# Kernel tuning notes

Measured on AMD Instinct MI355X. Metric: run time of the kernel, lower is better.

The kernel has to match this reference:

```python
import jax, jax.numpy as jnp
import numpy as np

DMODEL = 1024
N_EXPERTS = 16
EXPERT_SIZE = 256
K = 4


def setup_inputs() -> dict:
    key = jax.random.key(0)
    k1, k2, k3, k4 = jax.random.split(key, 4)
    std_sel = 1.0 / np.sqrt(DMODEL)
    std_val = 1.0 / np.sqrt(N_EXPERTS * EXPERT_SIZE)
    return {
        "x": jax.random.normal(k1, (4, 2048, DMODEL), dtype=jnp.float32),
        "expert_sel": jax.random.normal(k2, (N_EXPERTS, DMODEL), dtype=jnp.float32) * std_sel,
        "keys": jax.random.normal(k3, (N_EXPERTS, DMODEL, EXPERT_SIZE), dtype=jnp.float32) * std_sel,
        "values": jax.random.normal(k4, (N_EXPERTS, EXPERT_SIZE, DMODEL), dtype=jnp.float32) * std_val,
        "route_scale": jnp.ones((1,), dtype=jnp.float32),
    }


def reference(x, expert_sel, keys, values, route_scale):
    # Routing: sigmoid gating, top-k selection (eval mode: no dropout/bias balancing)
    sel_logits = jnp.einsum("btd,ed->bte", x, expert_sel)  # [B,T,E]
    sel_probs = jax.nn.sigmoid(sel_logits)
    _, sel_index = jax.lax.top_k(sel_probs, K)  # [B,T,K]
    sel_val = jnp.take_along_axis(sel_probs, sel_index, axis=-1)  # [B,T,K]
    sel_val = sel_val / jnp.clip(sel_val.sum(-1, keepdims=True), 1e-9)
    sel_val = sel_val * route_scale  # route_scale shape [1] broadcasts
    # Dense all-expert FFN (as in original), then gather top-k and combine
    scores_all = jax.nn.relu(jnp.einsum("btd,edh->bteh", x, keys))  # [B,T,E,H]
    values_all = jnp.einsum("bteh,ehv->btev", scores_all, values)   # [B,T,E,V]
    sel_idx_exp = sel_index[..., None]  # [B,T,K,1]
    selected = jnp.take_along_axis(values_all, sel_idx_exp, axis=2)  # [B,T,K,V]
    out = (selected * sel_val[..., None]).sum(axis=2)  # [B,T,V]
    return out
```

## Files before the change

### kernel.cpp

```cpp
#include <hip/hip_runtime.h>
#include <math.h>


constexpr int NTOK = 8192;
constexpr int DM   = 1024;
constexpr int NE   = 16;
constexpr int EH   = 256;
constexpr int TK   = 4;
constexpr int CAP  = 8192;
constexpr int BM   = 128;

typedef __attribute__((ext_vector_type(8))) short short8;
typedef __attribute__((ext_vector_type(4))) float f32x4;

#define MFMA16(a, b, c) __builtin_amdgcn_mfma_f32_16x16x32_bf16(a, b, c, 0, 0, 0)
#define VMCNT(n) asm volatile("s_waitcnt vmcnt(" #n ")" ::: "memory")
#define LGKM0    asm volatile("s_waitcnt lgkmcnt(0)" ::: "memory")
#define SBAR     __builtin_amdgcn_s_barrier()
#define SCHED0   __builtin_amdgcn_sched_barrier(0)

__device__ __forceinline__ void gload_lds16(const void* g, void* l) {
    __builtin_amdgcn_global_load_lds(
        (const __attribute__((address_space(1))) void*)g,
        (__attribute__((address_space(3))) void*)l, 16, 0, 0);
}

__device__ __forceinline__ unsigned short f2bf(float f) {
    union { float f; unsigned int u; } x; x.f = f;
    unsigned int r = x.u + 0x7fffu + ((x.u >> 16) & 1u);
    return (unsigned short)(r >> 16);
}
__device__ __forceinline__ float bf2f(unsigned short b) {
    union { unsigned int u; float f; } x; x.u = ((unsigned int)b) << 16;
    return x.f;
}

__global__ __launch_bounds__(256) void route_conv_kernel(
    const float* __restrict__ x, const float* __restrict__ esel,
    const float* __restrict__ rscale,
    unsigned short* __restrict__ xb,
    int4* __restrict__ sel4, float* __restrict__ wtk)
{
    __shared__ float Es[NE * DM];
    int tid = threadIdx.x;

    {
        const float4* src = (const float4*)esel;
        float4* dst = (float4*)Es;
        #pragma unroll
        for (int j = 0; j < 16; ++j) dst[tid + j * 256] = src[tid + j * 256];
    }
    __syncthreads();

    int t    = blockIdx.x * 8 + (tid >> 5);
    int l32  = tid & 31;

    float acc[NE];
    #pragma unroll
    for (int e = 0; e < NE; ++e) acc[e] = 0.f;

    const float4* x4 = (const float4*)(x + (size_t)t * DM);
    const float4* E4 = (const float4*)Es;
    #pragma unroll
    for (int i4 = 0; i4 < 8; ++i4) {
        int d4 = i4 * 32 + l32;
        float4 xv = x4[d4];
        ushort4 cb = { f2bf(xv.x), f2bf(xv.y), f2bf(xv.z), f2bf(xv.w) };
        *(ushort4*)(xb + (size_t)t * DM + d4 * 4) = cb;
        #pragma unroll
        for (int e = 0; e < NE; ++e) {
            float4 wv = E4[e * 256 + d4];
            acc[e] = fmaf(xv.x, wv.x, acc[e]);
            acc[e] = fmaf(xv.y, wv.y, acc[e]);
            acc[e] = fmaf(xv.z, wv.z, acc[e]);
            acc[e] = fmaf(xv.w, wv.w, acc[e]);
        }
    }

    #pragma unroll
    for (int off = 16; off; off >>= 1)
        #pragma unroll
        for (int e = 0; e < NE; ++e)
            acc[e] += __shfl_xor(acc[e], off, 32);

    if (l32 == 0) {
        float p[NE];
        #pragma unroll
        for (int e = 0; e < NE; ++e) p[e] = 1.0f / (1.0f + expf(-acc[e]));

        int   sel_e[TK];
        float sel_p[TK];
        float sum = 0.f;
        #pragma unroll
        for (int k = 0; k < TK; ++k) {
            float best = -INFINITY; int be = NE;
            #pragma unroll
            for (int e = 0; e < NE; ++e) {
                bool take = p[e] > best;
                best = take ? p[e] : best;
                be   = take ? e    : be;
            }
            sel_e[k] = be; sel_p[k] = best; sum += best;
            #pragma unroll
            for (int e = 0; e < NE; ++e) p[e] = (e == be) ? -INFINITY : p[e];
        }

        float wsc = rscale[0] / fmaxf(sum, 1e-9f);
        int4 s = { sel_e[0], sel_e[1], sel_e[2], sel_e[3] };
        sel4[t] = s;
        float4 wv = { sel_p[0] * wsc, sel_p[1] * wsc,
                      sel_p[2] * wsc, sel_p[3] * wsc };
        *(float4*)(wtk + t * TK) = wv;
    }
}

__global__ __launch_bounds__(1024) void compact_kernel(
    const int4* __restrict__ sel4, int* __restrict__ counts,
    int* __restrict__ lpk)
{
    __shared__ int wsum[16];
    int e    = blockIdx.x;
    int tid  = threadIdx.x;
    int w    = tid >> 6;
    int lane = tid & 63;

    int base = 0;
    for (int c = 0; c < NTOK; c += 1024) {
        int t = c + tid;
        int4 s = sel4[t];
        int k = -1;
        if      (s.x == e) k = 0;
        else if (s.y == e) k = 1;
        else if (s.z == e) k = 2;
        else if (s.w == e) k = 3;
        unsigned long long m = __ballot(k >= 0);
        int rank = __popcll(m & ((1ull << lane) - 1ull));
        if (lane == 63) wsum[w] = __popcll(m);
        __syncthreads();
        int prefix = 0, total = 0;
        #pragma unroll
        for (int i = 0; i < 16; ++i) {
            int v = wsum[i];
            prefix += (i < w) ? v : 0;
            total  += v;
        }
        if (k >= 0) lpk[e * CAP + base + prefix + rank] = t * TK + k;
        base += total;
        __syncthreads();
    }
    if (tid == 0) counts[e] = base;
}

__global__ __launch_bounds__(256) void trans_kernel(
    const float* __restrict__ in, unsigned short* __restrict__ outp, int R, int C)
{
    __shared__ float T[32][33];
    int e = blockIdx.z;
    int r0 = blockIdx.y * 32, c0 = blockIdx.x * 32;
    int ri = threadIdx.x >> 3, cq = threadIdx.x & 7;
    float4 v = *(const float4*)(in + ((size_t)e * R + r0 + ri) * C + c0 + cq * 4);
    T[ri][cq * 4 + 0] = v.x; T[ri][cq * 4 + 1] = v.y;
    T[ri][cq * 4 + 2] = v.z; T[ri][cq * 4 + 3] = v.w;
    __syncthreads();
    int ci = threadIdx.x >> 3, rq = threadIdx.x & 7;
    ushort4 o = { f2bf(T[rq * 4 + 0][ci]), f2bf(T[rq * 4 + 1][ci]),
                  f2bf(T[rq * 4 + 2][ci]), f2bf(T[rq * 4 + 3][ci]) };
    *(ushort4*)(outp + ((size_t)e * C + c0 + ci) * R + r0 + rq * 4) = o;
}

template<int USE_SCRATCH>
__global__ __launch_bounds__(512, 2) void ffn_kernel(
    const unsigned short* __restrict__ xb,
    const unsigned short* __restrict__ ktb,
    const unsigned short* __restrict__ vtb,
    const int* __restrict__ counts, const int* __restrict__ lpk,
    const float* __restrict__ wtk,
    unsigned short* __restrict__ scratch,
    float* __restrict__ out)
{
    constexpr int BUF  = 24576;
    constexpr int META = 3 * BUF + 65536;
    __shared__ __align__(16) char L[3 * BUF + 65536 + 1536];
    char* const Ss = L + 3 * BUF;
    int*   stok = (int*)(L + META);
    int*   spk  = (int*)(L + META + 512);
    float* sw   = (float*)(L + META + 1024);

    int tid  = threadIdx.x;
    int lane = tid & 63;
    int w    = tid >> 6;
    int lm   = lane & 15;
    int q    = lane >> 4;
    int th   = w >> 2;
    int hq   = w & 3;

    int xp = blockIdx.x & 7;
    int j0 = blockIdx.x >> 3;
    int e0 = xp * 2;
    int c0 = counts[e0], c1 = counts[e0 + 1];
    int n0 = (c0 + BM - 1) >> 7;
    int ntot = n0 + ((c1 + BM - 1) >> 7);

    for (int jt = j0; jt < ntot; jt += 48) {
        int e, t0, cnt;
        if (jt < n0) { e = e0;     t0 = jt << 7;        cnt = c0; }
        else         { e = e0 + 1; t0 = (jt - n0) << 7; cnt = c1; }

        if (tid < BM) {
            int s = t0 + tid;
            if (s < cnt) {
                int pk = lpk[e * CAP + s];
                stok[tid] = pk >> 2; spk[tid] = pk; sw[tid] = wtk[pk];
            } else {
                stok[tid] = 0; spk[tid] = USE_SCRATCH ? (NTOK * TK) : 0; sw[tid] = 0.f;
            }
        }
        LGKM0;
        SBAR;
        SCHED0;

        int rowX = tid >> 2;
        int cb   = ((tid & 3) * 16) ^ (((rowX >> 1) & 3) << 4);
        const unsigned short* kbase = ktb + (size_t)e * EH * DM;
        const unsigned short* vbase = vtb + (size_t)e * DM * EH;
        const unsigned short* srcX  = xb + (size_t)stok[rowX] * DM + (cb >> 1);
        const unsigned short* srcK0 = kbase + (size_t)rowX * DM + (cb >> 1);
        const unsigned short* srcK1 = kbase + (size_t)(rowX + 128) * DM + (cb >> 1);
        const unsigned short* srcV0 = vbase + (size_t)rowX * EH + (cb >> 1);
        const unsigned short* srcV1 = vbase + (size_t)(rowX + 128) * EH + (cb >> 1);

        auto stage1 = [&](char* buf, int kc) {
            gload_lds16(srcX + kc,  buf + w * 1024);
            gload_lds16(srcK0 + kc, buf + 8192 + w * 1024);
            gload_lds16(srcK1 + kc, buf + 16384 + w * 1024);
        };
        auto stageV = [&](char* buf, int nb, int kc) {
            gload_lds16(srcV0 + nb * 256 * EH + kc, buf + w * 1024);
            gload_lds16(srcV1 + nb * 256 * EH + kc, buf + 8192 + w * 1024);
        };

        f32x4 zero = {0.f, 0.f, 0.f, 0.f};
        f32x4 acc[4][4];
        #pragma unroll
        for (int mi = 0; mi < 4; ++mi)
            #pragma unroll
            for (int ni = 0; ni < 4; ++ni) acc[mi][ni] = zero;

        auto comp1 = [&](const char* buf) {
            const char* Kb = buf + 8192;
            short8 a[4], bb[4];
            #pragma unroll
            for (int mi = 0; mi < 4; ++mi) {
                int row = th * 64 + mi * 16 + lm;
                a[mi] = *(const short8*)(buf + row * 64 +
                         ((q * 16) ^ (((row >> 1) & 3) << 4)));
            }
            #pragma unroll
            for (int ni = 0; ni < 4; ++ni) {
                int row = hq * 64 + ni * 16 + lm;
                bb[ni] = *(const short8*)(Kb + row * 64 +
                          ((q * 16) ^ (((row >> 1) & 3) << 4)));
            }
            #pragma unroll
            for (int mi = 0; mi < 4; ++mi)
                #pragma unroll
                for (int ni = 0; ni < 4; ++ni)
                    acc[mi][ni] = MFMA16(a[mi], bb[ni], acc[mi][ni]);
        };

        stage1(L, 0);
        stage1(L + BUF, 32);
        for (int n = 0; n < 30; ++n) {
            VMCNT(3); SBAR; SCHED0;
            stage1(L + ((n + 2) % 3) * BUF, (n + 2) * 32);
            __builtin_amdgcn_s_setprio(1);
            comp1(L + (n % 3) * BUF);
            __builtin_amdgcn_s_setprio(0);
        }
        VMCNT(3); SBAR; SCHED0;
        stageV(L + 2 * BUF, 0, 0);
        __builtin_amdgcn_s_setprio(1);
        comp1(L);
        __builtin_amdgcn_s_setprio(0);
        VMCNT(2); SBAR; SCHED0;
        stageV(L, 0, 32);
        __builtin_amdgcn_s_setprio(1);
        comp1(L + BUF);
        __builtin_amdgcn_s_setprio(0);

        #pragma unroll
        for (int mi = 0; mi < 4; ++mi)
            #pragma unroll
            for (int ni = 0; ni < 4; ++ni) {
                f32x4 v = acc[mi][ni];
                #pragma unroll
                for (int r = 0; r < 4; ++r) {
                    int row = th * 64 + mi * 16 + q * 4 + r;
                    int col = hq * 64 + ni * 16 + lm;
                    *(unsigned short*)(Ss + row * 512 +
                        ((col * 2) ^ ((row & 7) << 4))) = f2bf(fmaxf(v[r], 0.f));
                }
            }
        LGKM0;

        int   spk_[4][4];
        float sw_[4][4];
        int   stok_[4][4];
        #pragma unroll
        for (int mi = 0; mi < 4; ++mi)
            #pragma unroll
            for (int r = 0; r < 4; ++r) {
                int slot = th * 64 + mi * 16 + q * 4 + r;
                spk_[mi][r] = spk[slot];
                if (!USE_SCRATCH) { sw_[mi][r] = sw[slot]; stok_[mi][r] = stok[slot]; }
            }

        for (int nb = 0; nb < 4; ++nb) {
            f32x4 acc2[4][4];
            #pragma unroll
            for (int mi = 0; mi < 4; ++mi)
                #pragma unroll
                for (int ni = 0; ni < 4; ++ni) acc2[mi][ni] = zero;

            #pragma unroll
            for (int j2 = 0; j2 < 8; ++j2) {
                int u = nb * 8 + j2;
                if (u == 31) { VMCNT(0); } else { VMCNT(2); }
                SBAR; SCHED0;
                if (u < 30) {
                    int u2 = u + 2;
                    stageV(L + ((u + 1) % 3) * BUF, u2 >> 3, (u2 & 7) * 32);
                }
                const char* Vb = L + ((u + 2) % 3) * BUF;
                short8 a[4], bb[4];
                #pragma unroll
                for (int mi = 0; mi < 4; ++mi) {
                    int row = th * 64 + mi * 16 + lm;
                    a[mi] = *(const short8*)(Ss + row * 512 +
                             ((j2 * 64 + q * 16) ^ ((row & 7) << 4)));
                }
                #pragma unroll
                for (int ni = 0; ni < 4; ++ni) {
                    int row = hq * 64 + ni * 16 + lm;
                    bb[ni] = *(const short8*)(Vb + row * 64 +
                              ((q * 16) ^ (((row >> 1) & 3) << 4)));
                }
                __builtin_amdgcn_s_setprio(1);
                #pragma unroll
                for (int mi = 0; mi < 4; ++mi)
                    #pragma unroll
                    for (int ni = 0; ni < 4; ++ni)
                        acc2[mi][ni] = MFMA16(a[mi], bb[ni], acc2[mi][ni]);
                __builtin_amdgcn_s_setprio(0);
            }

            #pragma unroll
            for (int mi = 0; mi < 4; ++mi)
                #pragma unroll
                for (int ni = 0; ni < 4; ++ni) {
                    f32x4 v = acc2[mi][ni];
                    #pragma unroll
                    for (int r = 0; r < 4; ++r) {
                        int d = nb * 256 + hq * 64 + ni * 16 + lm;
                        if (USE_SCRATCH) {
                            scratch[(size_t)spk_[mi][r] * DM + d] = f2bf(v[r]);
                        } else {
                            atomicAdd(out + (size_t)stok_[mi][r] * DM + d,
                                      sw_[mi][r] * v[r]);
                        }
                    }
                }
        }
    }
}

__global__ __launch_bounds__(256) void combine_kernel(
    const unsigned short* __restrict__ scratch, const float* __restrict__ wtk,
    float* __restrict__ out)
{
    int t  = blockIdx.x * 2 + (threadIdx.x >> 7);
    int d0 = (threadIdx.x & 127) * 8;
    float o[8] = {0.f, 0.f, 0.f, 0.f, 0.f, 0.f, 0.f, 0.f};
    #pragma unroll
    for (int k = 0; k < TK; ++k) {
        float wv = wtk[t * TK + k];
        uint4 qv = *(const uint4*)(scratch + (size_t)(t * TK + k) * DM + d0);
        unsigned int us[4] = {qv.x, qv.y, qv.z, qv.w};
        #pragma unroll
        for (int j = 0; j < 4; ++j) {
            o[j * 2 + 0] = fmaf(wv, bf2f((unsigned short)(us[j] & 0xffff)), o[j * 2 + 0]);
            o[j * 2 + 1] = fmaf(wv, bf2f((unsigned short)(us[j] >> 16)),    o[j * 2 + 1]);
        }
    }
    float4 w0 = {o[0], o[1], o[2], o[3]}, w1 = {o[4], o[5], o[6], o[7]};
    *(float4*)(out + (size_t)t * DM + d0)     = w0;
    *(float4*)(out + (size_t)t * DM + d0 + 4) = w1;
}

extern "C" void kernel_launch(void* const* d_in, const int* in_sizes, int n_in,
                              void* d_out, int out_size, void* d_ws, size_t ws_size,
                              hipStream_t stream) {
    const float* x      = (const float*)d_in[0];
    const float* esel   = (const float*)d_in[1];
    const float* keys   = (const float*)d_in[2];
    const float* values = (const float*)d_in[3];
    const float* rscale = (const float*)d_in[4];
    float* out = (float*)d_out;

    char* ws = (char*)d_ws;
    size_t o = 0;
    auto alloc = [&](size_t sz) { size_t r = o; o = (o + sz + 255) & ~(size_t)255; return r; };
    size_t o_counts = alloc(NE * 4);
    size_t o_lpk    = alloc((size_t)NE * CAP * 4);
    size_t o_sel4   = alloc((size_t)NTOK * 16);
    size_t o_wtk    = alloc((size_t)NTOK * TK * 4);
    size_t o_xb     = alloc((size_t)NTOK * DM * 2);
    size_t o_ktb    = alloc((size_t)NE * EH * DM * 2);
    size_t o_vtb    = alloc((size_t)NE * DM * EH * 2);
    size_t o_scr    = alloc(((size_t)NTOK * TK + BM) * DM * 2);
    size_t need_full = o;

    int*            counts  = (int*)(ws + o_counts);
    int*            lpk     = (int*)(ws + o_lpk);
    int4*           sel4    = (int4*)(ws + o_sel4);
    float*          wtk     = (float*)(ws + o_wtk);
    unsigned short* xb      = (unsigned short*)(ws + o_xb);
    unsigned short* ktb     = (unsigned short*)(ws + o_ktb);
    unsigned short* vtb     = (unsigned short*)(ws + o_vtb);
    unsigned short* scratch = (unsigned short*)(ws + o_scr);

    bool use_scratch = ws_size >= need_full;

    if (!use_scratch)
        hipMemsetAsync(d_out, 0, (size_t)out_size * sizeof(float), stream);

    route_conv_kernel<<<NTOK / 8, 256, 0, stream>>>(x, esel, rscale, xb,
                                                    sel4, wtk);
    compact_kernel<<<NE, 1024, 0, stream>>>(sel4, counts, lpk);
    trans_kernel<<<dim3(EH / 32, DM / 32, NE), 256, 0, stream>>>(keys, ktb, DM, EH);
    trans_kernel<<<dim3(DM / 32, EH / 32, NE), 256, 0, stream>>>(values, vtb, EH, DM);

    if (use_scratch) {
        ffn_kernel<1><<<384, 512, 0, stream>>>(
            xb, ktb, vtb, counts, lpk, wtk, scratch, out);
        combine_kernel<<<NTOK / 2, 256, 0, stream>>>(scratch, wtk, out);
    } else {
        ffn_kernel<0><<<384, 512, 0, stream>>>(
            xb, ktb, vtb, counts, lpk, wtk, scratch, out);
    }
}
```

Measured before the change: 140.0 us.

## Pre-swizzle weights into MFMA fragment layout and load expert weights directly to registers

The transpose kernels now write keys and values in a fragment-major bf16 layout, so each wave can load its MFMA B operands straight from global memory into registers, with no LDS staging. The FFN kernel moves to 64-token tiles and 256-thread blocks, 512 blocks in total. Only X is staged through LDS, and K and V fragments are double-buffered in registers. Scratch is written in a permuted column order that the combine kernel undoes. The aim is to cut LDS traffic and barriers per k-step, at the cost of more redundant global or L2 reads of weights per tile, since each block reads the full expert weights for only 64 tokens.

```diff
diff --git a/kernel.cpp b/kernel.cpp
--- a/kernel.cpp
+++ b/kernel.cpp
@@ -8,14 +8,13 @@
 constexpr int EH   = 256;
 constexpr int TK   = 4;
 constexpr int CAP  = 8192;
-constexpr int BM   = 128;
+constexpr int BM   = 64;
 
 typedef __attribute__((ext_vector_type(8))) short short8;
 typedef __attribute__((ext_vector_type(4))) float f32x4;
 
 #define MFMA16(a, b, c) __builtin_amdgcn_mfma_f32_16x16x32_bf16(a, b, c, 0, 0, 0)
 #define VMCNT(n) asm volatile("s_waitcnt vmcnt(" #n ")" ::: "memory")
-#define LGKM0    asm volatile("s_waitcnt lgkmcnt(0)" ::: "memory")
 #define SBAR     __builtin_amdgcn_s_barrier()
 #define SCHED0   __builtin_amdgcn_sched_barrier(0)
 
@@ -151,7 +150,7 @@
     if (tid == 0) counts[e] = base;
 }
 
-__global__ __launch_bounds__(256) void trans_kernel(
+__global__ __launch_bounds__(256) void transF_kernel(
     const float* __restrict__ in, unsigned short* __restrict__ outp, int R, int C)
 {
     __shared__ float T[32][33];
@@ -163,48 +162,52 @@
     T[ri][cq * 4 + 2] = v.z; T[ri][cq * 4 + 3] = v.w;
     __syncthreads();
     int ci = threadIdx.x >> 3, rq = threadIdx.x & 7;
+    int row = c0 + ci;
+    int kb  = r0 + rq * 4;
+    int nk32 = R >> 5;
+    size_t chunk = (size_t)e * (C >> 4) * nk32 + (size_t)(row >> 4) * nk32 + (kb >> 5);
+    size_t off = chunk * 512 +
+                 (size_t)(((((kb >> 3) & 3) * 16 + (row & 15)) * 8) + (kb & 7));
     ushort4 o = { f2bf(T[rq * 4 + 0][ci]), f2bf(T[rq * 4 + 1][ci]),
                   f2bf(T[rq * 4 + 2][ci]), f2bf(T[rq * 4 + 3][ci]) };
-    *(ushort4*)(outp + ((size_t)e * C + c0 + ci) * R + r0 + rq * 4) = o;
+    *(ushort4*)(outp + off) = o;
 }
 
 template<int USE_SCRATCH>
-__global__ __launch_bounds__(512, 2) void ffn_kernel(
+__global__ __launch_bounds__(256) void ffn_kernel(
     const unsigned short* __restrict__ xb,
-    const unsigned short* __restrict__ ktb,
-    const unsigned short* __restrict__ vtb,
+    const unsigned short* __restrict__ ktbF,
+    const unsigned short* __restrict__ vtbF,
     const int* __restrict__ counts, const int* __restrict__ lpk,
     const float* __restrict__ wtk,
     unsigned short* __restrict__ scratch,
     float* __restrict__ out)
 {
-    constexpr int BUF  = 24576;
-    constexpr int META = 3 * BUF + 65536;
-    __shared__ __align__(16) char L[3 * BUF + 65536 + 1536];
-    char* const Ss = L + 3 * BUF;
-    int*   stok = (int*)(L + META);
-    int*   spk  = (int*)(L + META + 512);
-    float* sw   = (float*)(L + META + 1024);
+    __shared__ __align__(16) char L[12288 + 32768 + 768];
+    char* const Xb = L;
+    char* const Ss = L + 12288;
+    int*   stok = (int*)(L + 45056);
+    int*   spk  = (int*)(L + 45056 + 256);
+    float* sw   = (float*)(L + 45056 + 512);
 
     int tid  = threadIdx.x;
     int lane = tid & 63;
     int w    = tid >> 6;
     int lm   = lane & 15;
     int q    = lane >> 4;
-    int th   = w >> 2;
-    int hq   = w & 3;
+    int lane8 = lane * 8;
 
     int xp = blockIdx.x & 7;
     int j0 = blockIdx.x >> 3;
     int e0 = xp * 2;
     int c0 = counts[e0], c1 = counts[e0 + 1];
-    int n0 = (c0 + BM - 1) >> 7;
-    int ntot = n0 + ((c1 + BM - 1) >> 7);
-
-    for (int jt = j0; jt < ntot; jt += 48) {
+    int n0 = (c0 + BM - 1) >> 6;
+    int ntot = n0 + ((c1 + BM - 1) >> 6);
+
+    for (int jt = j0; jt < ntot; jt += 64) {
         int e, t0, cnt;
-        if (jt < n0) { e = e0;     t0 = jt << 7;        cnt = c0; }
-        else         { e = e0 + 1; t0 = (jt - n0) << 7; cnt = c1; }
+        if (jt < n0) { e = e0;     t0 = jt << 6;        cnt = c0; }
+        else         { e = e0 + 1; t0 = (jt - n0) << 6; cnt = c1; }
 
         if (tid < BM) {
             int s = t0 + tid;
@@ -215,28 +218,26 @@
                 stok[tid] = 0; spk[tid] = USE_SCRATCH ? (NTOK * TK) : 0; sw[tid] = 0.f;
             }
         }
-        LGKM0;
-        SBAR;
-        SCHED0;
+        __syncthreads();
 
         int rowX = tid >> 2;
         int cb   = ((tid & 3) * 16) ^ (((rowX >> 1) & 3) << 4);
-        const unsigned short* kbase = ktb + (size_t)e * EH * DM;
-        const unsigned short* vbase = vtb + (size_t)e * DM * EH;
-        const unsigned short* srcX  = xb + (size_t)stok[rowX] * DM + (cb >> 1);
-        const unsigned short* srcK0 = kbase + (size_t)rowX * DM + (cb >> 1);
-        const unsigned short* srcK1 = kbase + (size_t)(rowX + 128) * DM + (cb >> 1);
-        const unsigned short* srcV0 = vbase + (size_t)rowX * EH + (cb >> 1);
-        const unsigned short* srcV1 = vbase + (size_t)(rowX + 128) * EH + (cb >> 1);
-
-        auto stage1 = [&](char* buf, int kc) {
-            gload_lds16(srcX + kc,  buf + w * 1024);
-            gload_lds16(srcK0 + kc, buf + 8192 + w * 1024);
-            gload_lds16(srcK1 + kc, buf + 16384 + w * 1024);
+        const unsigned short* srcX = xb + (size_t)stok[rowX] * DM + (cb >> 1);
+        const unsigned short* kfe  = ktbF + (size_t)e * 262144;
+        const unsigned short* vfe  = vtbF + (size_t)e * 262144;
+        int w4  = w * 4;
+        int w16 = w * 16;
+
+        auto stageX = [&](int n) {
+            if (n < 32)
+                gload_lds16(srcX + n * 32, Xb + (n % 3) * 4096 + tid * 16);
         };
-        auto stageV = [&](char* buf, int nb, int kc) {
-            gload_lds16(srcV0 + nb * 256 * EH + kc, buf + w * 1024);
-            gload_lds16(srcV1 + nb * 256 * EH + kc, buf + 8192 + w * 1024);
+        auto loadK = [&](short8 (&kr)[4], int n) {
+            if (n < 32) {
+                #pragma unroll
+                for (int ni = 0; ni < 4; ++ni)
+                    kr[ni] = *(const short8*)(kfe + (((w4 + ni) * 32 + n) << 9) + lane8);
+            }
         };
 
         f32x4 zero = {0.f, 0.f, 0.f, 0.f};
@@ -246,47 +247,54 @@
             #pragma unroll
             for (int ni = 0; ni < 4; ++ni) acc[mi][ni] = zero;
 
-        auto comp1 = [&](const char* buf) {
-            const char* Kb = buf + 8192;
-            short8 a[4], bb[4];
+        short8 krA[4], krB[4];
+
+        stageX(0); stageX(1); loadK(krA, 0);
+        SCHED0;
+        loadK(krB, 1);
+        SCHED0;
+
+        auto step1 = [&](int n, short8 (&kr)[4]) {
+            if (n == 0)       { VMCNT(4); }
+            else if (n == 31) { VMCNT(0); }
+            else              { VMCNT(5); }
+            SBAR; SCHED0;
+            stageX(n + 2);
+            const char* XB = Xb + (n % 3) * 4096;
+            short8 a[4];
             #pragma unroll
             for (int mi = 0; mi < 4; ++mi) {
-                int row = th * 64 + mi * 16 + lm;
-                a[mi] = *(const short8*)(buf + row * 64 +
+                int row = mi * 16 + lm;
+                a[mi] = *(const short8*)(XB + row * 64 +
                          ((q * 16) ^ (((row >> 1) & 3) << 4)));
             }
-            #pragma unroll
-            for (int ni = 0; ni < 4; ++ni) {
-                int row = hq * 64 + ni * 16 + lm;
-                bb[ni] = *(const short8*)(Kb + row * 64 +
-                          ((q * 16) ^ (((row >> 1) & 3) << 4)));
-            }
+            __builtin_amdgcn_s_setprio(1);
             #pragma unroll
             for (int mi = 0; mi < 4; ++mi)
                 #pragma unroll
                 for (int ni = 0; ni < 4; ++ni)
-                    acc[mi][ni] = MFMA16(a[mi], bb[ni], acc[mi][ni]);
+                    acc[mi][ni] = MFMA16(a[mi], kr[ni], acc[mi][ni]);
+            __builtin_amdgcn_s_setprio(0);
+            loadK(kr, n + 2);
         };
 
-        stage1(L, 0);
-        stage1(L + BUF, 32);
-        for (int n = 0; n < 30; ++n) {
-            VMCNT(3); SBAR; SCHED0;
-            stage1(L + ((n + 2) % 3) * BUF, (n + 2) * 32);
-            __builtin_amdgcn_s_setprio(1);
-            comp1(L + (n % 3) * BUF);
-            __builtin_amdgcn_s_setprio(0);
-        }
-        VMCNT(3); SBAR; SCHED0;
-        stageV(L + 2 * BUF, 0, 0);
-        __builtin_amdgcn_s_setprio(1);
-        comp1(L);
-        __builtin_amdgcn_s_setprio(0);
-        VMCNT(2); SBAR; SCHED0;
-        stageV(L, 0, 32);
-        __builtin_amdgcn_s_setprio(1);
-        comp1(L + BUF);
-        __builtin_amdgcn_s_setprio(0);
+        #pragma unroll
+        for (int n = 0; n < 32; ++n) {
+            if (n & 1) step1(n, krB);
+            else       step1(n, krA);
+        }
+
+        int   spk_[4][4];
+        float sw_[4][4];
+        int   stok_[4][4];
+        #pragma unroll
+        for (int mi = 0; mi < 4; ++mi)
+            #pragma unroll
+            for (int r = 0; r < 4; ++r) {
+                int slot = mi * 16 + q * 4 + r;
+                spk_[mi][r] = spk[slot];
+                if (!USE_SCRATCH) { sw_[mi][r] = sw[slot]; stok_[mi][r] = stok[slot]; }
+            }
 
         #pragma unroll
         for (int mi = 0; mi < 4; ++mi)
@@ -295,81 +303,79 @@
                 f32x4 v = acc[mi][ni];
                 #pragma unroll
                 for (int r = 0; r < 4; ++r) {
-                    int row = th * 64 + mi * 16 + q * 4 + r;
-                    int col = hq * 64 + ni * 16 + lm;
+                    int row = mi * 16 + q * 4 + r;
+                    int col = w * 64 + ni * 16 + lm;
                     *(unsigned short*)(Ss + row * 512 +
                         ((col * 2) ^ ((row & 7) << 4))) = f2bf(fmaxf(v[r], 0.f));
                 }
             }
-        LGKM0;
-
-        int   spk_[4][4];
-        float sw_[4][4];
-        int   stok_[4][4];
-        #pragma unroll
-        for (int mi = 0; mi < 4; ++mi)
-            #pragma unroll
-            for (int r = 0; r < 4; ++r) {
-                int slot = th * 64 + mi * 16 + q * 4 + r;
-                spk_[mi][r] = spk[slot];
-                if (!USE_SCRATCH) { sw_[mi][r] = sw[slot]; stok_[mi][r] = stok[slot]; }
-            }
-
-        for (int nb = 0; nb < 4; ++nb) {
-            f32x4 acc2[4][4];
-            #pragma unroll
-            for (int mi = 0; mi < 4; ++mi)
-                #pragma unroll
-                for (int ni = 0; ni < 4; ++ni) acc2[mi][ni] = zero;
-
-            #pragma unroll
-            for (int j2 = 0; j2 < 8; ++j2) {
-                int u = nb * 8 + j2;
-                if (u == 31) { VMCNT(0); } else { VMCNT(2); }
-                SBAR; SCHED0;
-                if (u < 30) {
-                    int u2 = u + 2;
-                    stageV(L + ((u + 1) % 3) * BUF, u2 >> 3, (u2 & 7) * 32);
-                }
-                const char* Vb = L + ((u + 2) % 3) * BUF;
-                short8 a[4], bb[4];
-                #pragma unroll
-                for (int mi = 0; mi < 4; ++mi) {
-                    int row = th * 64 + mi * 16 + lm;
-                    a[mi] = *(const short8*)(Ss + row * 512 +
-                             ((j2 * 64 + q * 16) ^ ((row & 7) << 4)));
-                }
-                #pragma unroll
-                for (int ni = 0; ni < 4; ++ni) {
-                    int row = hq * 64 + ni * 16 + lm;
-                    bb[ni] = *(const short8*)(Vb + row * 64 +
-                              ((q * 16) ^ (((row >> 1) & 3) << 4)));
-                }
-                __builtin_amdgcn_s_setprio(1);
+        __syncthreads();
+
+        short8 vA[4], vB[4];
+        auto loadV = [&](short8 (&vr)[4], int u) {
+            if (u < 32) {
+                int d16b = w16 + ((u >> 3) << 2);
+                int kk = u & 7;
+                #pragma unroll
+                for (int ni = 0; ni < 4; ++ni)
+                    vr[ni] = *(const short8*)(vfe + ((((size_t)(d16b + ni)) * 8 + kk) << 9) + lane8);
+            }
+        };
+        loadV(vA, 0); loadV(vB, 1);
+
+        f32x4 acc2[4][4];
+        auto step2 = [&](int u, short8 (&vr)[4]) {
+            int kk = u & 7, nb = u >> 3;
+            if (kk == 0) {
                 #pragma unroll
                 for (int mi = 0; mi < 4; ++mi)
                     #pragma unroll
-                    for (int ni = 0; ni < 4; ++ni)
-                        acc2[mi][ni] = MFMA16(a[mi], bb[ni], acc2[mi][ni]);
-                __builtin_amdgcn_s_setprio(0);
-            }
-
+                    for (int ni = 0; ni < 4; ++ni) acc2[mi][ni] = zero;
+            }
+            short8 a2[4];
+            #pragma unroll
+            for (int mi = 0; mi < 4; ++mi) {
+                int row = mi * 16 + lm;
+                a2[mi] = *(const short8*)(Ss + row * 512 +
+                          ((kk * 64 + q * 16) ^ ((row & 7) << 4)));
+            }
+            __builtin_amdgcn_s_setprio(1);
             #pragma unroll
             for (int mi = 0; mi < 4; ++mi)
                 #pragma unroll
-                for (int ni = 0; ni < 4; ++ni) {
-                    f32x4 v = acc2[mi][ni];
+                for (int ni = 0; ni < 4; ++ni)
+                    acc2[mi][ni] = MFMA16(a2[mi], vr[ni], acc2[mi][ni]);
+            __builtin_amdgcn_s_setprio(0);
+            loadV(vr, u + 2);
+            if (kk == 7) {
+                #pragma unroll
+                for (int mi = 0; mi < 4; ++mi)
                     #pragma unroll
                     for (int r = 0; r < 4; ++r) {
-                        int d = nb * 256 + hq * 64 + ni * 16 + lm;
                         if (USE_SCRATCH) {
-                            scratch[(size_t)spk_[mi][r] * DM + d] = f2bf(v[r]);
+                            unsigned int lo = (unsigned int)f2bf(acc2[mi][0][r]) |
+                                              ((unsigned int)f2bf(acc2[mi][1][r]) << 16);
+                            unsigned int hi = (unsigned int)f2bf(acc2[mi][2][r]) |
+                                              ((unsigned int)f2bf(acc2[mi][3][r]) << 16);
+                            uint2 pv = { lo, hi };
+                            *(uint2*)(scratch + (size_t)spk_[mi][r] * DM +
+                                      (w4 + nb) * 64 + lm * 4) = pv;
                         } else {
-                            atomicAdd(out + (size_t)stok_[mi][r] * DM + d,
-                                      sw_[mi][r] * v[r]);
+                            #pragma unroll
+                            for (int ni = 0; ni < 4; ++ni) {
+                                int d = w * 256 + nb * 64 + ni * 16 + lm;
+                                atomicAdd(out + (size_t)stok_[mi][r] * DM + d,
+                                          sw_[mi][r] * acc2[mi][ni][r]);
+                            }
                         }
                     }
-                }
+            }
+        };
+
+        #pragma unroll
+        for (int u = 0; u < 32; ++u) {
+            if (u & 1) step2(u, vB);
+            else       step2(u, vA);
         }
     }
 }
@@ -378,23 +384,29 @@
     const unsigned short* __restrict__ scratch, const float* __restrict__ wtk,
     float* __restrict__ out)
 {
-    int t  = blockIdx.x * 2 + (threadIdx.x >> 7);
-    int d0 = (threadIdx.x & 127) * 8;
+    int t   = blockIdx.x * 2 + (threadIdx.x >> 7);
+    int l   = threadIdx.x & 127;
+    int blk = l >> 3;
+    int lm2 = l & 7;
     float o[8] = {0.f, 0.f, 0.f, 0.f, 0.f, 0.f, 0.f, 0.f};
     #pragma unroll
     for (int k = 0; k < TK; ++k) {
         float wv = wtk[t * TK + k];
-        uint4 qv = *(const uint4*)(scratch + (size_t)(t * TK + k) * DM + d0);
-        unsigned int us[4] = {qv.x, qv.y, qv.z, qv.w};
+        uint4 qv = *(const uint4*)(scratch + (size_t)(t * TK + k) * DM +
+                                   blk * 64 + lm2 * 8);
+        unsigned int us[4] = { qv.x, qv.y, qv.z, qv.w };
         #pragma unroll
         for (int j = 0; j < 4; ++j) {
             o[j * 2 + 0] = fmaf(wv, bf2f((unsigned short)(us[j] & 0xffff)), o[j * 2 + 0]);
             o[j * 2 + 1] = fmaf(wv, bf2f((unsigned short)(us[j] >> 16)),    o[j * 2 + 1]);
         }
     }
-    float4 w0 = {o[0], o[1], o[2], o[3]}, w1 = {o[4], o[5], o[6], o[7]};
-    *(float4*)(out + (size_t)t * DM + d0)     = w0;
-    *(float4*)(out + (size_t)t * DM + d0 + 4) = w1;
+    float* ob = out + (size_t)t * DM + blk * 64 + 2 * lm2;
+    #pragma unroll
+    for (int ni = 0; ni < 4; ++ni) {
+        float2 f2 = { o[ni], o[ni + 4] };
+        *(float2*)(ob + ni * 16) = f2;
+    }
 }
 
 extern "C" void kernel_launch(void* const* d_in, const int* in_sizes, int n_in,
@@ -425,8 +437,8 @@
     int4*           sel4    = (int4*)(ws + o_sel4);
     float*          wtk     = (float*)(ws + o_wtk);
     unsigned short* xb      = (unsigned short*)(ws + o_xb);
-    unsigned short* ktb     = (unsigned short*)(ws + o_ktb);
-    unsigned short* vtb     = (unsigned short*)(ws + o_vtb);
+    unsigned short* ktbF    = (unsigned short*)(ws + o_ktb);
+    unsigned short* vtbF    = (unsigned short*)(ws + o_vtb);
     unsigned short* scratch = (unsigned short*)(ws + o_scr);
 
     bool use_scratch = ws_size >= need_full;
@@ -437,15 +449,15 @@
     route_conv_kernel<<<NTOK / 8, 256, 0, stream>>>(x, esel, rscale, xb,
                                                     sel4, wtk);
     compact_kernel<<<NE, 1024, 0, stream>>>(sel4, counts, lpk);
-    trans_kernel<<<dim3(EH / 32, DM / 32, NE), 256, 0, stream>>>(keys, ktb, DM, EH);
-    trans_kernel<<<dim3(DM / 32, EH / 32, NE), 256, 0, stream>>>(values, vtb, EH, DM);
+    transF_kernel<<<dim3(EH / 32, DM / 32, NE), 256, 0, stream>>>(keys, ktbF, DM, EH);
+    transF_kernel<<<dim3(DM / 32, EH / 32, NE), 256, 0, stream>>>(values, vtbF, EH, DM);
 
     if (use_scratch) {
-        ffn_kernel<1><<<384, 512, 0, stream>>>(
-            xb, ktb, vtb, counts, lpk, wtk, scratch, out);
+        ffn_kernel<1><<<512, 256, 0, stream>>>(
+            xb, ktbF, vtbF, counts, lpk, wtk, scratch, out);
         combine_kernel<<<NTOK / 2, 256, 0, stream>>>(scratch, wtk, out);
     } else {
-        ffn_kernel<0><<<384, 512, 0, stream>>>(
-            xb, ktb, vtb, counts, lpk, wtk, scratch, out);
-    }
-}
+        ffn_kernel<0><<<512, 256, 0, stream>>>(
+            xb, ktbF, vtbF, counts, lpk, wtk, scratch, out);
+    }
+}
```

New measurement: 138.2 us. No clear change (-1.3%).
